# Kernel tuning notes

Hardware: AMD Instinct MI355X
Metric: run time of the kernel (lower is better)

## Reference

```python
import jax, jax.numpy as jnp
import numpy as np

BS, LQ = 16, 300
D, NH = 256, 8
HD = D // NH
NLAYERS, DFF = 6, 1024
NLVL, NPTS = 4, 4
SUMP = NLVL * NPTS  # total sampling points per head
SPATIAL = [(80, 80), (40, 40), (20, 20), (10, 10)]
LEN_V = sum(h * w for h, w in SPATIAL)  # 8500
OFFSET_SCALE = 0.5


def layer_norm(x, g, b, eps=1e-5):
    m = jnp.mean(x, -1, keepdims=True)
    v = jnp.mean((x - m) ** 2, -1, keepdims=True)
    return (x - m) * jax.lax.rsqrt(v + eps) * g + b


def bilinear_gather(v, loc, Hs, Ws):
    # v: [bs, nh, Hs*Ws, hd]; loc: [bs, nh, N, 2] in [0,1] (x, y)
    # grid_sample bilinear, align_corners=False, zero padding
    x = loc[..., 0] * Ws - 0.5
    y = loc[..., 1] * Hs - 0.5
    x0 = jnp.floor(x); y0 = jnp.floor(y)
    x1 = x0 + 1.0; y1 = y0 + 1.0
    wx1 = x - x0; wx0 = 1.0 - wx1
    wy1 = y - y0; wy0 = 1.0 - wy1

    def corner(xi, yi, w):
        valid = (xi >= 0) & (xi <= Ws - 1) & (yi >= 0) & (yi <= Hs - 1)
        idx = (jnp.clip(yi, 0, Hs - 1) * Ws + jnp.clip(xi, 0, Ws - 1)).astype(jnp.int32)
        g = jnp.take_along_axis(v, idx[..., None], axis=2)  # [bs,nh,N,hd]
        return g * (w * valid)[..., None]

    return (corner(x0, y0, wx0 * wy0) + corner(x1, y0, wx1 * wy0)
            + corner(x0, y1, wx0 * wy1) + corner(x1, y1, wx1 * wy1))


def ms_deform_attn(value, loc, attn_w):
    # value [bs,LenV,D]; loc [bs,Lq,nh,SUMP,2]; attn_w [bs,Lq,nh,SUMP]
    bs, Lq = loc.shape[:2]
    v = value.reshape(bs, -1, NH, HD).transpose(0, 2, 1, 3)  # [bs,nh,LenV,hd]
    sizes = [h * w for h, w in SPATIAL]
    offs = np.cumsum([0] + sizes)
    outs = []
    for lvl, (Hs, Ws) in enumerate(SPATIAL):
        v_l = v[:, :, offs[lvl]:offs[lvl + 1], :]
        loc_l = loc[:, :, :, lvl * NPTS:(lvl + 1) * NPTS, :]
        loc_l = loc_l.transpose(0, 2, 1, 3, 4).reshape(bs, NH, Lq * NPTS, 2)
        s = bilinear_gather(v_l, loc_l, Hs, Ws).reshape(bs, NH, Lq, NPTS, HD)
        outs.append(s)
    samp = jnp.concatenate(outs, axis=3)  # [bs,nh,Lq,SUMP,hd]
    w = attn_w.transpose(0, 2, 1, 3)[..., None]
    out = jnp.sum(samp * w, axis=3)  # [bs,nh,Lq,hd]
    return out.transpose(0, 2, 1, 3).reshape(bs, Lq, D)


def mha(q_in, k_in, v_in, Wqkv, bqkv, Wo, bo):
    # torch nn.MultiheadAttention (batch_first), no dropout, no mask
    bs, Lq, _ = q_in.shape
    Wq, Wk, Wv = jnp.split(Wqkv, 3, axis=0)
    bq, bk, bv = jnp.split(bqkv, 3)
    q = (q_in @ Wq.T + bq).reshape(bs, Lq, NH, HD)
    k = (k_in @ Wk.T + bk).reshape(bs, -1, NH, HD)
    v = (v_in @ Wv.T + bv).reshape(bs, -1, NH, HD)
    scores = jnp.einsum('bqhd,bkhd->bhqk', q, k) / jnp.sqrt(jnp.float32(HD))
    a = jax.nn.softmax(scores, axis=-1)
    o = jnp.einsum('bhqk,bkhd->bqhd', a, v).reshape(bs, Lq, D)
    return o @ Wo.T + bo


def _forward(target, reference_points, value, query_pos_embed,
             attn_Wqkv, attn_bqkv, attn_Wo, attn_bo, n1_g, n1_b,
             so_W, so_b, aw_W, aw_b, g_W, g_b, gn_g, gn_b,
             l1_W, l1_b, l2_W, l2_b, n3_g, n3_b):
    bs, Lq = target.shape[:2]
    # num_points_scale = 1/n_points per point (all levels use NPTS points)
    nps = jnp.full((SUMP, 1), 1.0 / NPTS, dtype=target.dtype)
    t = target
    for i in range(NLAYERS):
        # self-attention
        q = t + query_pos_embed
        t2 = mha(q, q, t, attn_Wqkv[i], attn_bqkv[i], attn_Wo[i], attn_bo[i])
        t = layer_norm(t + t2, n1_g[i], n1_b[i])
        # MS deformable cross-attention (4-dim reference_points branch)
        qc = t + query_pos_embed
        so = (qc @ so_W[i].T + so_b[i]).reshape(bs, Lq, NH, SUMP, 2)
        aw = jax.nn.softmax((qc @ aw_W[i].T + aw_b[i]).reshape(bs, Lq, NH, SUMP), axis=-1)
        ref = reference_points[:, :, None, None, :]  # [bs,Lq,1,1,4]
        loc = ref[..., :2] + so * nps * ref[..., 2:] * OFFSET_SCALE
        t2 = ms_deform_attn(value, loc, aw)
        # gateway fusion
        gates = jax.nn.sigmoid(jnp.concatenate([t, t2], -1) @ g_W[i].T + g_b[i])
        g1, g2 = jnp.split(gates, 2, axis=-1)
        t = layer_norm(g1 * t + g2 * t2, gn_g[i], gn_b[i])
        # FFN
        t2 = jax.nn.relu(t @ l1_W[i].T + l1_b[i]) @ l2_W[i].T + l2_b[i]
        t = layer_norm(jnp.clip(t + t2, -65504.0, 65504.0), n3_g[i], n3_b[i])
    return t


def setup_inputs() -> dict:
    key = jax.random.key(0)
    ks = iter(jax.random.split(key, 40))

    def rn(shape, s=0.02):
        return jax.random.normal(next(ks), shape, dtype=jnp.float32) * s

    inp = {
        'target': jax.random.normal(next(ks), (BS, LQ, D), dtype=jnp.float32),
        'reference_points': jax.random.uniform(next(ks), (BS, LQ, 4), dtype=jnp.float32) * 0.5 + 0.25,
        'value': jax.random.normal(next(ks), (BS, LEN_V, D), dtype=jnp.float32),
        'query_pos_embed': jax.random.normal(next(ks), (BS, LQ, D), dtype=jnp.float32),
        'attn_Wqkv': rn((NLAYERS, 3 * D, D)),
        'attn_bqkv': jnp.zeros((NLAYERS, 3 * D), jnp.float32),
        'attn_Wo': rn((NLAYERS, D, D)),
        'attn_bo': jnp.zeros((NLAYERS, D), jnp.float32),
        'n1_g': jnp.ones((NLAYERS, D), jnp.float32),
        'n1_b': jnp.zeros((NLAYERS, D), jnp.float32),
        'so_W': rn((NLAYERS, NH * SUMP * 2, D)),
        'so_b': rn((NLAYERS, NH * SUMP * 2), 0.5),
        'aw_W': rn((NLAYERS, NH * SUMP, D)),
        'aw_b': jnp.zeros((NLAYERS, NH * SUMP), jnp.float32),
        'g_W': rn((NLAYERS, 2 * D, 2 * D)),
        'g_b': jnp.zeros((NLAYERS, 2 * D), jnp.float32),
        'gn_g': jnp.ones((NLAYERS, D), jnp.float32),
        'gn_b': jnp.zeros((NLAYERS, D), jnp.float32),
        'l1_W': rn((NLAYERS, DFF, D)),
        'l1_b': jnp.zeros((NLAYERS, DFF), jnp.float32),
        'l2_W': rn((NLAYERS, D, DFF)),
        'l2_b': jnp.zeros((NLAYERS, D), jnp.float32),
        'n3_g': jnp.ones((NLAYERS, D), jnp.float32),
        'n3_b': jnp.zeros((NLAYERS, D), jnp.float32),
    }
    return inp


def reference(target, reference_points, value, query_pos_embed,
              attn_Wqkv, attn_bqkv, attn_Wo, attn_bo, n1_g, n1_b,
              so_W, so_b, aw_W, aw_b, g_W, g_b, gn_g, gn_b,
              l1_W, l1_b, l2_W, l2_b, n3_g, n3_b):
    return _forward(target, reference_points, value, query_pos_embed,
                    attn_Wqkv, attn_bqkv, attn_Wo, attn_bo, n1_g, n1_b,
                    so_W, so_b, aw_W, aw_b, g_W, g_b, gn_g, gn_b,
                    l1_W, l1_b, l2_W, l2_b, n3_g, n3_b)
```

## Files before the change

kernel.cpp:

```cpp
#include <hip/hip_runtime.h>

#define BS 16
#define LQ 300
#define D 256
#define NH 8
#define HD 32
#define DFF 1024
#define ROWS (BS*LQ)
#define LEN_V 8500

typedef __attribute__((ext_vector_type(8))) short short8;
typedef __attribute__((ext_vector_type(4))) float f32x4;

__device__ __forceinline__ uint32_t bf16r(float x)
{
    const uint32_t u = __float_as_uint(x);
    return (u + 0x7fffu + ((u >> 16) & 1u)) >> 16;
}
__device__ __forceinline__ float lof(uint32_t p) { return __uint_as_float(p << 16); }
__device__ __forceinline__ float hif(uint32_t p) { return __uint_as_float(p & 0xffff0000u); }

template<int ACT>
__global__ __launch_bounds__(256)
void gemm_f32(const float* __restrict__ A, const float* __restrict__ Aalt,
              int bnsplit_a, int lda,
              const float* __restrict__ A2, int lda2, int ksplit,
              const float* __restrict__ W, const float* __restrict__ W2, int bnw,
              const float* __restrict__ bias, const float* __restrict__ bias2,
              float* __restrict__ C, int ldc, float* __restrict__ C2, int ldc2,
              int K)
{
    __shared__ __align__(16) unsigned short As[64*64];
    __shared__ __align__(16) unsigned short Bs[64*64];
    const int tid  = threadIdx.x;
    const int bm   = blockIdx.x, bn = blockIdx.y;
    const int lane = tid & 63;
    const int w    = tid >> 6;
    const int wm   = (w >> 1) * 32, wn = (w & 1) * 32;
    const int fr   = lane & 15;
    const int fq   = lane >> 4;

    const int srow = tid >> 2;
    const int sg   = tid & 3;

    if (bn >= bnsplit_a) A = Aalt;
    const float* Wb; const float* biasb; float* Cb; int ldcb; int colbase;
    if (bn < bnw) {
        Wb = W  + (size_t)bn*64*K;        biasb = bias;
        Cb = C;  ldcb = ldc;  colbase = bn*64;
    } else {
        Wb = W2 + (size_t)(bn-bnw)*64*K;  biasb = bias2;
        Cb = C2; ldcb = ldc2; colbase = (bn-bnw)*64;
    }

    f32x4 acc[2][2] = {};

    for (int k0 = 0; k0 < K; k0 += 64) {
        float4 a0[2], a1[2], w0[2], w1[2];
#pragma unroll
        for (int p = 0; p < 2; ++p) {
            const int slot = sg + 4*p;
            const int kg   = k0 + slot*8;
            const float* Asrc = (A2 != nullptr && kg >= ksplit)
                ? (A2 + (size_t)(bm*64 + srow)*lda2 + (kg - ksplit))
                : (A  + (size_t)(bm*64 + srow)*lda  + kg);
            a0[p] = *reinterpret_cast<const float4*>(Asrc);
            a1[p] = *reinterpret_cast<const float4*>(Asrc + 4);
            const float* Wsrc = Wb + (size_t)srow*K + kg;
            w0[p] = *reinterpret_cast<const float4*>(Wsrc);
            w1[p] = *reinterpret_cast<const float4*>(Wsrc + 4);
        }
        __syncthreads();
#pragma unroll
        for (int p = 0; p < 2; ++p) {
            const int slot = (sg + 4*p) ^ (srow & 7);
            uint32_t pk[4];
            pk[0] = bf16r(a0[p].x) | (bf16r(a0[p].y) << 16);
            pk[1] = bf16r(a0[p].z) | (bf16r(a0[p].w) << 16);
            pk[2] = bf16r(a1[p].x) | (bf16r(a1[p].y) << 16);
            pk[3] = bf16r(a1[p].z) | (bf16r(a1[p].w) << 16);
            *reinterpret_cast<uint4*>(&As[srow*64 + slot*8]) =
                make_uint4(pk[0], pk[1], pk[2], pk[3]);
            pk[0] = bf16r(w0[p].x) | (bf16r(w0[p].y) << 16);
            pk[1] = bf16r(w0[p].z) | (bf16r(w0[p].w) << 16);
            pk[2] = bf16r(w1[p].x) | (bf16r(w1[p].y) << 16);
            pk[3] = bf16r(w1[p].z) | (bf16r(w1[p].w) << 16);
            *reinterpret_cast<uint4*>(&Bs[srow*64 + slot*8]) =
                make_uint4(pk[0], pk[1], pk[2], pk[3]);
        }
        __syncthreads();
#pragma unroll
        for (int ks = 0; ks < 2; ++ks) {
            short8 af[2], bf[2];
#pragma unroll
            for (int fm = 0; fm < 2; ++fm) {
                const int row = wm + fm*16 + fr;
                const int slot = (ks*4 + fq) ^ (row & 7);
                af[fm] = *reinterpret_cast<const short8*>(&As[row*64 + slot*8]);
            }
#pragma unroll
            for (int fn = 0; fn < 2; ++fn) {
                const int row = wn + fn*16 + fr;
                const int slot = (ks*4 + fq) ^ (row & 7);
                bf[fn] = *reinterpret_cast<const short8*>(&Bs[row*64 + slot*8]);
            }
#pragma unroll
            for (int fm = 0; fm < 2; ++fm)
#pragma unroll
                for (int fn = 0; fn < 2; ++fn)
                    acc[fm][fn] = __builtin_amdgcn_mfma_f32_16x16x32_bf16(
                        af[fm], bf[fn], acc[fm][fn], 0, 0, 0);
        }
    }

#pragma unroll
    for (int fm = 0; fm < 2; ++fm)
#pragma unroll
        for (int fn = 0; fn < 2; ++fn) {
            const int coll = wn + fn*16 + fr;
            const float bia = biasb[colbase + coll];
#pragma unroll
            for (int r = 0; r < 4; ++r) {
                const int row = bm*64 + wm + fm*16 + fq*4 + r;
                float v = acc[fm][fn][r] + bia;
                if (ACT == 1) v = fmaxf(v, 0.f);
                if (ACT == 2) v = 1.f / (1.f + __expf(-v));
                Cb[(size_t)row*ldcb + colbase + coll] = v;
            }
        }
}

__global__ __launch_bounds__(256)
void prep0(const float* __restrict__ target, const float* __restrict__ pos,
           float* __restrict__ t, float* __restrict__ q)
{
    const size_t idx = (size_t)blockIdx.x*256 + threadIdx.x;
    const float v = target[idx];
    t[idx] = v;
    q[idx] = v + pos[idx];
}

__global__ __launch_bounds__(256)
void mha_block(const float* __restrict__ qkv, float* __restrict__ o)
{
    const int blk = blockIdx.x;
    const int quarter = blk & 3;
    const int bh = blk >> 2;
    const int b = bh >> 3, h = bh & 7;
    const int tid = threadIdx.x;
    const int lane = tid & 63;
    const int w = tid >> 6;

    __shared__ uint32_t Kp[16][320];
    __shared__ uint32_t Vp[150][32];
    __shared__ float    ws[4][304];
    const float* base = qkv + (size_t)b * LQ * 768;
    const int hc = h * 32;

    for (int idx = tid; idx < 300*16; idx += 256) {
        const int j = idx >> 4, d2 = idx & 15;
        const float2 kv = *reinterpret_cast<const float2*>(base + (size_t)j*768 + 256 + hc + 2*d2);
        Kp[d2][j] = (bf16r(kv.y) << 16) | bf16r(kv.x);
    }
    for (int idx = tid; idx < 16*20; idx += 256)
        Kp[idx/20][300 + idx%20] = 0;
    for (int idx = tid; idx < 150*32; idx += 256) {
        const int jp = idx >> 5, d = idx & 31;
        const float lo = base[(size_t)(2*jp  )*768 + 512 + hc + d];
        const float hi = base[(size_t)(2*jp+1)*768 + 512 + hc + d];
        Vp[jp][d] = (bf16r(hi) << 16) | bf16r(lo);
    }
    __syncthreads();

    const float scale = 0.17677669529663687f;
    const int qbase = quarter * 75;
    for (int il = w; il < 75; il += 4) {
        const int iq = qbase + il;
        const float2* qrow = reinterpret_cast<const float2*>(base + (size_t)iq*768 + hc);

        float s0=0.f, s1=0.f, s2=0.f, s3=0.f, s4=0.f;
#pragma unroll
        for (int d2 = 0; d2 < 16; ++d2) {
            const float2 q2 = qrow[d2];
            uint32_t k;
            k = Kp[d2][lane      ]; s0 += lof(k)*q2.x + hif(k)*q2.y;
            k = Kp[d2][lane +  64]; s1 += lof(k)*q2.x + hif(k)*q2.y;
            k = Kp[d2][lane + 128]; s2 += lof(k)*q2.x + hif(k)*q2.y;
            k = Kp[d2][lane + 192]; s3 += lof(k)*q2.x + hif(k)*q2.y;
            k = Kp[d2][lane + 256]; s4 += lof(k)*q2.x + hif(k)*q2.y;
        }
        s0 *= scale; s1 *= scale; s2 *= scale; s3 *= scale;
        s4 = (lane < 44) ? s4*scale : -3e38f;

        float m = fmaxf(fmaxf(fmaxf(s0,s1), fmaxf(s2,s3)), s4);
#pragma unroll
        for (int off = 32; off; off >>= 1) m = fmaxf(m, __shfl_xor(m, off));
        const float e0 = __expf(s0-m), e1 = __expf(s1-m), e2 = __expf(s2-m), e3 = __expf(s3-m);
        const float e4 = (lane < 44) ? __expf(s4-m) : 0.f;
        float sum = e0+e1+e2+e3+e4;
#pragma unroll
        for (int off = 32; off; off >>= 1) sum += __shfl_xor(sum, off);
        const float inv = 1.f / sum;
        ws[w][lane      ] = e0;
        ws[w][lane +  64] = e1;
        ws[w][lane + 128] = e2;
        ws[w][lane + 192] = e3;
        if (lane < 44) ws[w][lane + 256] = e4;

        const int half = lane >> 5, d = lane & 31;
        float acc = 0.f;
#pragma unroll 5
        for (int jp = half*75; jp < half*75 + 75; ++jp) {
            const float2 w2 = *reinterpret_cast<const float2*>(&ws[w][2*jp]);
            const uint32_t v2 = Vp[jp][d];
            acc += lof(v2)*w2.x + hif(v2)*w2.y;
        }
        acc += __shfl_down(acc, 32);
        if (lane < 32)
            o[((size_t)(b*LQ + iq))*256 + hc + d] = acc * inv;
    }
}

__device__ __forceinline__ float blk_sum(float v, float* red)
{
#pragma unroll
    for (int off = 32; off; off >>= 1) v += __shfl_down(v, off, 64);
    const int lane = threadIdx.x & 63, w = threadIdx.x >> 6;
    if (lane == 0) red[w] = v;
    __syncthreads();
    const float s = red[0] + red[1] + red[2] + red[3];
    __syncthreads();
    return s;
}

__global__ __launch_bounds__(256)
void ln_res_pos(const float* __restrict__ t, const float* __restrict__ t2,
                const float* __restrict__ g, const float* __restrict__ bb,
                const float* __restrict__ pos,
                float* __restrict__ t_out, float* __restrict__ q_out)
{
    __shared__ float red[4];
    const size_t idx = (size_t)blockIdx.x*256 + threadIdx.x;
    const float x = t[idx] + t2[idx];
    const float mean = blk_sum(x, red) * (1.f/256.f);
    const float c = x - mean;
    const float var = blk_sum(c*c, red) * (1.f/256.f);
    const float y = c * rsqrtf(var + 1e-5f) * g[threadIdx.x] + bb[threadIdx.x];
    t_out[idx] = y;
    q_out[idx] = y + pos[idx];
}

__global__ __launch_bounds__(256)
void gate_ln(const float* __restrict__ t, const float* __restrict__ t2,
             const float* __restrict__ gates,
             const float* __restrict__ g, const float* __restrict__ bb,
             float* __restrict__ t_out)
{
    __shared__ float red[4];
    const int row = blockIdx.x, dd = threadIdx.x;
    const size_t idx = (size_t)row*256 + dd;
    const float g1 = gates[(size_t)row*512 + dd];
    const float g2 = gates[(size_t)row*512 + 256 + dd];
    const float x = g1 * t[idx] + g2 * t2[idx];
    const float mean = blk_sum(x, red) * (1.f/256.f);
    const float c = x - mean;
    const float var = blk_sum(c*c, red) * (1.f/256.f);
    t_out[idx] = c * rsqrtf(var + 1e-5f) * g[dd] + bb[dd];
}

__global__ __launch_bounds__(256)
void ln_clip(const float* __restrict__ t, const float* __restrict__ t2,
             const float* __restrict__ g, const float* __restrict__ bb,
             const float* __restrict__ pos,
             float* __restrict__ outp, float* __restrict__ q_out)
{
    __shared__ float red[4];
    const size_t idx = (size_t)blockIdx.x*256 + threadIdx.x;
    float x = t[idx] + t2[idx];
    x = fminf(fmaxf(x, -65504.f), 65504.f);
    const float mean = blk_sum(x, red) * (1.f/256.f);
    const float c = x - mean;
    const float var = blk_sum(c*c, red) * (1.f/256.f);
    const float y = c * rsqrtf(var + 1e-5f) * g[threadIdx.x] + bb[threadIdx.x];
    outp[idx] = y;
    if (q_out != nullptr) q_out[idx] = y + pos[idx];
}

__global__ __launch_bounds__(256)
void deform_attn(const float* __restrict__ value, const float* __restrict__ refp,
                 const float* __restrict__ so, const float* __restrict__ awl,
                 float* __restrict__ outp)
{
    const int bq = blockIdx.x;
    const int b  = bq / LQ;
    const int tid = threadIdx.x;
    __shared__ int   s_idx[128][4];
    __shared__ float s_w[128][4];
    if (tid < 128) {
        const int hp = tid;
        const int p  = hp & 15;
        const int lvl = p >> 2;
        const float Wl = (lvl == 0) ? 80.f : (lvl == 1) ? 40.f : (lvl == 2) ? 20.f : 10.f;
        const float Hl = Wl;
        const int off  = (lvl == 0) ? 0 : (lvl == 1) ? 6400 : (lvl == 2) ? 8000 : 8400;
        const float logit = awl[(size_t)bq*128 + hp];
        float m = logit;
#pragma unroll
        for (int o = 8; o; o >>= 1) m = fmaxf(m, __shfl_xor(m, o, 16));
        const float e = __expf(logit - m);
        float ssum = e;
#pragma unroll
        for (int o = 8; o; o >>= 1) ssum += __shfl_xor(ssum, o, 16);
        const float a = e / ssum;

        const float cx = refp[bq*4+0], cy = refp[bq*4+1];
        const float rw = refp[bq*4+2], rh = refp[bq*4+3];
        const float lx = cx + so[(size_t)bq*256 + hp*2    ] * rw * 0.125f;
        const float ly = cy + so[(size_t)bq*256 + hp*2 + 1] * rh * 0.125f;
        const float x = lx * Wl - 0.5f;
        const float y = ly * Hl - 0.5f;
        const float x0 = floorf(x), y0 = floorf(y);
        const float wx1 = x - x0, wx0 = 1.f - wx1;
        const float wy1 = y - y0, wy0 = 1.f - wy1;
        const float xs[2]  = {x0, x0 + 1.f}, ys[2]  = {y0, y0 + 1.f};
        const float wxs[2] = {wx0, wx1},     wys[2] = {wy0, wy1};
#pragma unroll
        for (int cyi = 0; cyi < 2; ++cyi)
#pragma unroll
            for (int cxi = 0; cxi < 2; ++cxi) {
                const float xi = xs[cxi], yi = ys[cyi];
                const bool valid = (xi >= 0.f) && (xi <= Wl - 1.f) &&
                                   (yi >= 0.f) && (yi <= Hl - 1.f);
                const float xc = fminf(fmaxf(xi, 0.f), Wl - 1.f);
                const float yc = fminf(fmaxf(yi, 0.f), Hl - 1.f);
                const int c = cyi*2 + cxi;
                s_idx[hp][c] = (int)(yc*Wl + xc) + off;
                s_w[hp][c]   = valid ? (wxs[cxi]*wys[cyi]*a) : 0.f;
            }
    }
    __syncthreads();
    const int h = tid >> 5, d = tid & 31;
    const int col = h*32 + d;
    const float* vb = value + (size_t)b * LEN_V * 256;
    float acc = 0.f;
#pragma unroll
    for (int p = 0; p < 16; ++p) {
        const int hp = (h << 4) | p;
#pragma unroll
        for (int c = 0; c < 4; ++c)
            acc += s_w[hp][c] * vb[(size_t)s_idx[hp][c]*256 + col];
    }
    outp[(size_t)bq*256 + col] = acc;
}

extern "C" void kernel_launch(void* const* d_in, const int* in_sizes, int n_in,
                              void* d_out, int out_size, void* d_ws, size_t ws_size,
                              hipStream_t stream)
{
    (void)in_sizes; (void)n_in; (void)out_size; (void)ws_size;
    const float* target = (const float*)d_in[0];
    const float* refp   = (const float*)d_in[1];
    const float* value  = (const float*)d_in[2];
    const float* qpos   = (const float*)d_in[3];
    const float* Wqkv   = (const float*)d_in[4];
    const float* bqkv   = (const float*)d_in[5];
    const float* Wo     = (const float*)d_in[6];
    const float* bo     = (const float*)d_in[7];
    const float* n1g    = (const float*)d_in[8];
    const float* n1b    = (const float*)d_in[9];
    const float* soW    = (const float*)d_in[10];
    const float* sob    = (const float*)d_in[11];
    const float* awW    = (const float*)d_in[12];
    const float* awb    = (const float*)d_in[13];
    const float* gW     = (const float*)d_in[14];
    const float* gb     = (const float*)d_in[15];
    const float* gng    = (const float*)d_in[16];
    const float* gnb    = (const float*)d_in[17];
    const float* l1W    = (const float*)d_in[18];
    const float* l1b    = (const float*)d_in[19];
    const float* l2W    = (const float*)d_in[20];
    const float* l2b    = (const float*)d_in[21];
    const float* n3g    = (const float*)d_in[22];
    const float* n3b    = (const float*)d_in[23];

    float* p = (float*)d_ws;
    float* t_buf = p;  p += (size_t)ROWS*D;
    float* q_buf = p;  p += (size_t)ROWS*D;
    float* qkv   = p;
    float* o_buf = qkv + (size_t)ROWS*768;
    float* hid   = qkv;
    p += (size_t)ROWS*(768 + 256);
    float* t2    = p;  p += (size_t)ROWS*D;
    float* so_b  = p;  p += (size_t)ROWS*D;
    float* aw_b  = p;  p += (size_t)ROWS*128;
    float* gates = p;  p += (size_t)ROWS*512;

    prep0<<<ROWS, 256, 0, stream>>>(target, qpos, t_buf, q_buf);

    for (int i = 0; i < 6; ++i) {
        const float* Wqkv_i = Wqkv + (size_t)i*768*256;
        const float* bqkv_i = bqkv + (size_t)i*768;
        const float* Wo_i   = Wo   + (size_t)i*256*256;
        const float* bo_i   = bo   + (size_t)i*256;
        const float* n1g_i  = n1g  + (size_t)i*256;
        const float* n1b_i  = n1b  + (size_t)i*256;
        const float* soW_i  = soW  + (size_t)i*256*256;
        const float* sob_i  = sob  + (size_t)i*256;
        const float* awW_i  = awW  + (size_t)i*128*256;
        const float* awb_i  = awb  + (size_t)i*128;
        const float* gW_i   = gW   + (size_t)i*512*512;
        const float* gb_i   = gb   + (size_t)i*512;
        const float* gng_i  = gng  + (size_t)i*256;
        const float* gnb_i  = gnb  + (size_t)i*256;
        const float* l1W_i  = l1W  + (size_t)i*1024*256;
        const float* l1b_i  = l1b  + (size_t)i*1024;
        const float* l2W_i  = l2W  + (size_t)i*256*1024;
        const float* l2b_i  = l2b  + (size_t)i*256;
        const float* n3g_i  = n3g  + (size_t)i*256;
        const float* n3b_i  = n3b  + (size_t)i*256;

        gemm_f32<0><<<dim3(75, 12), 256, 0, stream>>>(
            q_buf, t_buf, 8, 256,  nullptr, 0, 0,
            Wqkv_i, nullptr, 999,  bqkv_i, nullptr,
            qkv, 768, nullptr, 0,  256);
        mha_block<<<BS*NH*4, 256, 0, stream>>>(qkv, o_buf);
        gemm_f32<0><<<dim3(75, 4), 256, 0, stream>>>(
            o_buf, o_buf, 999, 256,  nullptr, 0, 0,
            Wo_i, nullptr, 999,  bo_i, nullptr,
            t2, 256, nullptr, 0,  256);
        ln_res_pos<<<ROWS, 256, 0, stream>>>(t_buf, t2, n1g_i, n1b_i, qpos, t_buf, q_buf);

        gemm_f32<0><<<dim3(75, 6), 256, 0, stream>>>(
            q_buf, q_buf, 999, 256,  nullptr, 0, 0,
            soW_i, awW_i, 4,  sob_i, awb_i,
            so_b, 256, aw_b, 128,  256);
        deform_attn<<<ROWS, 256, 0, stream>>>(value, refp, so_b, aw_b, t2);

        gemm_f32<2><<<dim3(75, 8), 256, 0, stream>>>(
            t_buf, t_buf, 999, 256,  t2, 256, 256,
            gW_i, nullptr, 999,  gb_i, nullptr,
            gates, 512, nullptr, 0,  512);
        gate_ln<<<ROWS, 256, 0, stream>>>(t_buf, t2, gates, gng_i, gnb_i, t_buf);

        gemm_f32<1><<<dim3(75, 16), 256, 0, stream>>>(
            t_buf, t_buf, 999, 256,  nullptr, 0, 0,
            l1W_i, nullptr, 999,  l1b_i, nullptr,
            hid, 1024, nullptr, 0,  256);
        gemm_f32<0><<<dim3(75, 4), 256, 0, stream>>>(
            hid, hid, 999, 1024,  nullptr, 0, 0,
            l2W_i, nullptr, 999,  l2b_i, nullptr,
            t2, 256, nullptr, 0,  1024);
        ln_clip<<<ROWS, 256, 0, stream>>>(t_buf, t2, n3g_i, n3b_i, qpos,
                                          (i == 5) ? (float*)d_out : t_buf,
                                          (i < 5) ? q_buf : nullptr);
    }
}
```

Before: 1.309 ms.

## Widen GEMM N-tile to 128 and gather deformable values from bf16 copy

The GEMM kernel is templated on its N-tile width, and the QKV, gate and FFN1 projections now use 128-wide tiles. This halves their block counts and reuses each A tile across more columns. Separately, the value tensor is converted once per call into a bf16 copy in workspace, so the deformable-attention gather reads half the bytes on every layer. The workspace is also compacted by aliasing intermediate buffers so that the bf16 copy fits, with a fallback to the fp32 path when the workspace is too small. This adds one conversion pass and lowers precision on the gathered values.

Result: slower. 1.424 ms (+8.8%).

```diff
diff --git a/kernel.cpp b/kernel.cpp
--- a/kernel.cpp
+++ b/kernel.cpp
@@ -11,6 +11,7 @@
 
 typedef __attribute__((ext_vector_type(8))) short short8;
 typedef __attribute__((ext_vector_type(4))) float f32x4;
+typedef unsigned short ushort_t;
 
 __device__ __forceinline__ uint32_t bf16r(float x)
 {
@@ -20,7 +21,7 @@
 __device__ __forceinline__ float lof(uint32_t p) { return __uint_as_float(p << 16); }
 __device__ __forceinline__ float hif(uint32_t p) { return __uint_as_float(p & 0xffff0000u); }
 
-template<int ACT>
+template<int ACT, int BN>
 __global__ __launch_bounds__(256)
 void gemm_f32(const float* __restrict__ A, const float* __restrict__ Aalt,
               int bnsplit_a, int lda,
@@ -30,84 +31,97 @@
               float* __restrict__ C, int ldc, float* __restrict__ C2, int ldc2,
               int K)
 {
-    __shared__ __align__(16) unsigned short As[64*64];
-    __shared__ __align__(16) unsigned short Bs[64*64];
+    constexpr int NFR = BN / 32;
+    constexpr int BP  = BN / 32;
+    __shared__ __align__(16) ushort_t As[64*64];
+    __shared__ __align__(16) ushort_t Bs[BN*64];
     const int tid  = threadIdx.x;
     const int bm   = blockIdx.x, bn = blockIdx.y;
     const int lane = tid & 63;
     const int w    = tid >> 6;
-    const int wm   = (w >> 1) * 32, wn = (w & 1) * 32;
+    const int wm   = (w >> 1) * 32, wn = (w & 1) * (BN/2);
     const int fr   = lane & 15;
     const int fq   = lane >> 4;
 
-    const int srow = tid >> 2;
-    const int sg   = tid & 3;
+    const int srow = tid >> 3;
+    const int slot = tid & 7;
 
     if (bn >= bnsplit_a) A = Aalt;
     const float* Wb; const float* biasb; float* Cb; int ldcb; int colbase;
     if (bn < bnw) {
-        Wb = W  + (size_t)bn*64*K;        biasb = bias;
-        Cb = C;  ldcb = ldc;  colbase = bn*64;
+        Wb = W  + (size_t)bn*BN*K;        biasb = bias;
+        Cb = C;  ldcb = ldc;  colbase = bn*BN;
     } else {
-        Wb = W2 + (size_t)(bn-bnw)*64*K;  biasb = bias2;
-        Cb = C2; ldcb = ldc2; colbase = (bn-bnw)*64;
-    }
-
-    f32x4 acc[2][2] = {};
+        Wb = W2 + (size_t)(bn-bnw)*BN*K;  biasb = bias2;
+        Cb = C2; ldcb = ldc2; colbase = (bn-bnw)*BN;
+    }
+
+    f32x4 acc[2][NFR] = {};
 
     for (int k0 = 0; k0 < K; k0 += 64) {
-        float4 a0[2], a1[2], w0[2], w1[2];
-#pragma unroll
-        for (int p = 0; p < 2; ++p) {
-            const int slot = sg + 4*p;
-            const int kg   = k0 + slot*8;
+        const int kg = k0 + slot*8;
+        float4 a0[2], a1[2], b0[BP], b1[BP];
+#pragma unroll
+        for (int pa = 0; pa < 2; ++pa) {
+            const int row = srow + 32*pa;
             const float* Asrc = (A2 != nullptr && kg >= ksplit)
-                ? (A2 + (size_t)(bm*64 + srow)*lda2 + (kg - ksplit))
-                : (A  + (size_t)(bm*64 + srow)*lda  + kg);
-            a0[p] = *reinterpret_cast<const float4*>(Asrc);
-            a1[p] = *reinterpret_cast<const float4*>(Asrc + 4);
-            const float* Wsrc = Wb + (size_t)srow*K + kg;
-            w0[p] = *reinterpret_cast<const float4*>(Wsrc);
-            w1[p] = *reinterpret_cast<const float4*>(Wsrc + 4);
+                ? (A2 + (size_t)(bm*64 + row)*lda2 + (kg - ksplit))
+                : (A  + (size_t)(bm*64 + row)*lda  + kg);
+            a0[pa] = *reinterpret_cast<const float4*>(Asrc);
+            a1[pa] = *reinterpret_cast<const float4*>(Asrc + 4);
+        }
+#pragma unroll
+        for (int pb = 0; pb < BP; ++pb) {
+            const int row = srow + 32*pb;
+            const float* Wsrc = Wb + (size_t)row*K + kg;
+            b0[pb] = *reinterpret_cast<const float4*>(Wsrc);
+            b1[pb] = *reinterpret_cast<const float4*>(Wsrc + 4);
         }
         __syncthreads();
 #pragma unroll
-        for (int p = 0; p < 2; ++p) {
-            const int slot = (sg + 4*p) ^ (srow & 7);
+        for (int pa = 0; pa < 2; ++pa) {
+            const int row = srow + 32*pa;
+            const int sl  = slot ^ (row & 7);
             uint32_t pk[4];
-            pk[0] = bf16r(a0[p].x) | (bf16r(a0[p].y) << 16);
-            pk[1] = bf16r(a0[p].z) | (bf16r(a0[p].w) << 16);
-            pk[2] = bf16r(a1[p].x) | (bf16r(a1[p].y) << 16);
-            pk[3] = bf16r(a1[p].z) | (bf16r(a1[p].w) << 16);
-            *reinterpret_cast<uint4*>(&As[srow*64 + slot*8]) =
+            pk[0] = bf16r(a0[pa].x) | (bf16r(a0[pa].y) << 16);
+            pk[1] = bf16r(a0[pa].z) | (bf16r(a0[pa].w) << 16);
+            pk[2] = bf16r(a1[pa].x) | (bf16r(a1[pa].y) << 16);
+            pk[3] = bf16r(a1[pa].z) | (bf16r(a1[pa].w) << 16);
+            *reinterpret_cast<uint4*>(&As[row*64 + sl*8]) =
                 make_uint4(pk[0], pk[1], pk[2], pk[3]);
-            pk[0] = bf16r(w0[p].x) | (bf16r(w0[p].y) << 16);
-            pk[1] = bf16r(w0[p].z) | (bf16r(w0[p].w) << 16);
-            pk[2] = bf16r(w1[p].x) | (bf16r(w1[p].y) << 16);
-            pk[3] = bf16r(w1[p].z) | (bf16r(w1[p].w) << 16);
-            *reinterpret_cast<uint4*>(&Bs[srow*64 + slot*8]) =
+        }
+#pragma unroll
+        for (int pb = 0; pb < BP; ++pb) {
+            const int row = srow + 32*pb;
+            const int sl  = slot ^ (row & 7);
+            uint32_t pk[4];
+            pk[0] = bf16r(b0[pb].x) | (bf16r(b0[pb].y) << 16);
+            pk[1] = bf16r(b0[pb].z) | (bf16r(b0[pb].w) << 16);
+            pk[2] = bf16r(b1[pb].x) | (bf16r(b1[pb].y) << 16);
+            pk[3] = bf16r(b1[pb].z) | (bf16r(b1[pb].w) << 16);
+            *reinterpret_cast<uint4*>(&Bs[row*64 + sl*8]) =
                 make_uint4(pk[0], pk[1], pk[2], pk[3]);
         }
         __syncthreads();
 #pragma unroll
         for (int ks = 0; ks < 2; ++ks) {
-            short8 af[2], bf[2];
+            short8 af[2], bf[NFR];
 #pragma unroll
             for (int fm = 0; fm < 2; ++fm) {
                 const int row = wm + fm*16 + fr;
-                const int slot = (ks*4 + fq) ^ (row & 7);
-                af[fm] = *reinterpret_cast<const short8*>(&As[row*64 + slot*8]);
+                const int sl  = (ks*4 + fq) ^ (row & 7);
+                af[fm] = *reinterpret_cast<const short8*>(&As[row*64 + sl*8]);
             }
 #pragma unroll
-            for (int fn = 0; fn < 2; ++fn) {
+            for (int fn = 0; fn < NFR; ++fn) {
                 const int row = wn + fn*16 + fr;
-                const int slot = (ks*4 + fq) ^ (row & 7);
-                bf[fn] = *reinterpret_cast<const short8*>(&Bs[row*64 + slot*8]);
+                const int sl  = (ks*4 + fq) ^ (row & 7);
+                bf[fn] = *reinterpret_cast<const short8*>(&Bs[row*64 + sl*8]);
             }
 #pragma unroll
             for (int fm = 0; fm < 2; ++fm)
 #pragma unroll
-                for (int fn = 0; fn < 2; ++fn)
+                for (int fn = 0; fn < NFR; ++fn)
                     acc[fm][fn] = __builtin_amdgcn_mfma_f32_16x16x32_bf16(
                         af[fm], bf[fn], acc[fm][fn], 0, 0, 0);
         }
@@ -116,7 +130,7 @@
 #pragma unroll
     for (int fm = 0; fm < 2; ++fm)
 #pragma unroll
-        for (int fn = 0; fn < 2; ++fn) {
+        for (int fn = 0; fn < NFR; ++fn) {
             const int coll = wn + fn*16 + fr;
             const float bia = biasb[colbase + coll];
 #pragma unroll
@@ -138,6 +152,17 @@
     const float v = target[idx];
     t[idx] = v;
     q[idx] = v + pos[idx];
+}
+
+__global__ __launch_bounds__(256)
+void cvt_flat4(const float* __restrict__ src, ushort_t* __restrict__ dst, int n4)
+{
+    for (int i = blockIdx.x*256 + threadIdx.x; i < n4; i += gridDim.x*256) {
+        const float4 v = reinterpret_cast<const float4*>(src)[i];
+        ushort_t o[4] = {(ushort_t)bf16r(v.x), (ushort_t)bf16r(v.y),
+                         (ushort_t)bf16r(v.z), (ushort_t)bf16r(v.w)};
+        *reinterpret_cast<uint2*>(dst + (size_t)i*4) = *reinterpret_cast<uint2*>(o);
+    }
 }
 
 __global__ __launch_bounds__(256)
@@ -286,8 +311,9 @@
     if (q_out != nullptr) q_out[idx] = y + pos[idx];
 }
 
-__global__ __launch_bounds__(256)
-void deform_attn(const float* __restrict__ value, const float* __restrict__ refp,
+template<int VBF>
+__global__ __launch_bounds__(256)
+void deform_attn(const void* __restrict__ value_p, const float* __restrict__ refp,
                  const float* __restrict__ so, const float* __restrict__ awl,
                  float* __restrict__ outp)
 {
@@ -341,14 +367,26 @@
     __syncthreads();
     const int h = tid >> 5, d = tid & 31;
     const int col = h*32 + d;
-    const float* vb = value + (size_t)b * LEN_V * 256;
     float acc = 0.f;
-#pragma unroll
-    for (int p = 0; p < 16; ++p) {
-        const int hp = (h << 4) | p;
-#pragma unroll
-        for (int c = 0; c < 4; ++c)
-            acc += s_w[hp][c] * vb[(size_t)s_idx[hp][c]*256 + col];
+    if (VBF) {
+        const ushort_t* vb = (const ushort_t*)value_p + (size_t)b * LEN_V * 256;
+#pragma unroll
+        for (int p = 0; p < 16; ++p) {
+            const int hp = (h << 4) | p;
+#pragma unroll
+            for (int c = 0; c < 4; ++c)
+                acc += s_w[hp][c] *
+                       __uint_as_float(((uint32_t)vb[(size_t)s_idx[hp][c]*256 + col]) << 16);
+        }
+    } else {
+        const float* vb = (const float*)value_p + (size_t)b * LEN_V * 256;
+#pragma unroll
+        for (int p = 0; p < 16; ++p) {
+            const int hp = (h << 4) | p;
+#pragma unroll
+            for (int c = 0; c < 4; ++c)
+                acc += s_w[hp][c] * vb[(size_t)s_idx[hp][c]*256 + col];
+        }
     }
     outp[(size_t)bq*256 + col] = acc;
 }
@@ -357,7 +395,7 @@
                               void* d_out, int out_size, void* d_ws, size_t ws_size,
                               hipStream_t stream)
 {
-    (void)in_sizes; (void)n_in; (void)out_size; (void)ws_size;
+    (void)in_sizes; (void)n_in; (void)out_size;
     const float* target = (const float*)d_in[0];
     const float* refp   = (const float*)d_in[1];
     const float* value  = (const float*)d_in[2];
@@ -386,15 +424,23 @@
     float* p = (float*)d_ws;
     float* t_buf = p;  p += (size_t)ROWS*D;
     float* q_buf = p;  p += (size_t)ROWS*D;
-    float* qkv   = p;
-    float* o_buf = qkv + (size_t)ROWS*768;
-    float* hid   = qkv;
-    p += (size_t)ROWS*(768 + 256);
+    float* R     = p;  p += (size_t)ROWS*1024;
     float* t2    = p;  p += (size_t)ROWS*D;
-    float* so_b  = p;  p += (size_t)ROWS*D;
-    float* aw_b  = p;  p += (size_t)ROWS*128;
-    float* gates = p;  p += (size_t)ROWS*512;
-
+
+    float* qkv   = R;
+    float* o_buf = R + (size_t)ROWS*768;
+    float* so_b  = R;
+    float* aw_b  = R + (size_t)ROWS*256;
+    float* gates = R;
+    float* hid   = R;
+
+    const size_t base_bytes = (size_t)((char*)p - (char*)d_ws);
+    const size_t val_elems  = (size_t)BS*LEN_V*256;
+    ushort_t* val_bf = (ushort_t*)p;
+    const bool use_vbf = (ws_size >= base_bytes + val_elems*2);
+
+    if (use_vbf)
+        cvt_flat4<<<2048, 256, 0, stream>>>(value, val_bf, (int)(val_elems/4));
     prep0<<<ROWS, 256, 0, stream>>>(target, qpos, t_buf, q_buf);
 
     for (int i = 0; i < 6; ++i) {
@@ -419,34 +465,37 @@
         const float* n3g_i  = n3g  + (size_t)i*256;
         const float* n3b_i  = n3b  + (size_t)i*256;
 
-        gemm_f32<0><<<dim3(75, 12), 256, 0, stream>>>(
-            q_buf, t_buf, 8, 256,  nullptr, 0, 0,
+        gemm_f32<0,128><<<dim3(75, 6), 256, 0, stream>>>(
+            q_buf, t_buf, 4, 256,  nullptr, 0, 0,
             Wqkv_i, nullptr, 999,  bqkv_i, nullptr,
             qkv, 768, nullptr, 0,  256);
         mha_block<<<BS*NH*4, 256, 0, stream>>>(qkv, o_buf);
-        gemm_f32<0><<<dim3(75, 4), 256, 0, stream>>>(
+        gemm_f32<0,64><<<dim3(75, 4), 256, 0, stream>>>(
             o_buf, o_buf, 999, 256,  nullptr, 0, 0,
             Wo_i, nullptr, 999,  bo_i, nullptr,
             t2, 256, nullptr, 0,  256);
         ln_res_pos<<<ROWS, 256, 0, stream>>>(t_buf, t2, n1g_i, n1b_i, qpos, t_buf, q_buf);
 
-        gemm_f32<0><<<dim3(75, 6), 256, 0, stream>>>(
+        gemm_f32<0,64><<<dim3(75, 6), 256, 0, stream>>>(
             q_buf, q_buf, 999, 256,  nullptr, 0, 0,
             soW_i, awW_i, 4,  sob_i, awb_i,
             so_b, 256, aw_b, 128,  256);
-        deform_attn<<<ROWS, 256, 0, stream>>>(value, refp, so_b, aw_b, t2);
-
-        gemm_f32<2><<<dim3(75, 8), 256, 0, stream>>>(
+        if (use_vbf)
+            deform_attn<1><<<ROWS, 256, 0, stream>>>(val_bf, refp, so_b, aw_b, t2);
+        else
+            deform_attn<0><<<ROWS, 256, 0, stream>>>(value, refp, so_b, aw_b, t2);
+
+        gemm_f32<2,128><<<dim3(75, 4), 256, 0, stream>>>(
             t_buf, t_buf, 999, 256,  t2, 256, 256,
             gW_i, nullptr, 999,  gb_i, nullptr,
             gates, 512, nullptr, 0,  512);
         gate_ln<<<ROWS, 256, 0, stream>>>(t_buf, t2, gates, gng_i, gnb_i, t_buf);
 
-        gemm_f32<1><<<dim3(75, 16), 256, 0, stream>>>(
+        gemm_f32<1,128><<<dim3(75, 8), 256, 0, stream>>>(
             t_buf, t_buf, 999, 256,  nullptr, 0, 0,
             l1W_i, nullptr, 999,  l1b_i, nullptr,
             hid, 1024, nullptr, 0,  256);
-        gemm_f32<0><<<dim3(75, 4), 256, 0, stream>>>(
+        gemm_f32<0,64><<<dim3(75, 4), 256, 0, stream>>>(
             hid, hid, 999, 1024,  nullptr, 0, 0,
             l2W_i, nullptr, 999,  l2b_i, nullptr,
             t2, 256, nullptr, 0,  1024);
```
